# Kernel tuning notes

Hardware: AMD Instinct MI355X
Metric: run time of the kernel (lower is better)

Reference implementation:

```python
import jax, jax.numpy as jnp
import numpy as np

N_NODES = 100000
N_EDGES = 1600000
D_IN = 64
D_HID = 64


def setup_inputs() -> dict:
    key = jax.random.key(0)
    ks = jax.random.split(key, 9)
    feat = jax.random.uniform(ks[0], (N_NODES, D_IN), dtype=jnp.float32) + 1e-3
    edge_index = jax.random.randint(ks[1], (2, N_EDGES), 0, N_NODES, dtype=jnp.int64)
    edge_vals = jax.random.uniform(ks[2], (N_EDGES,), dtype=jnp.float32) + 1e-3
    W1 = jax.random.normal(ks[3], (D_IN, D_HID), dtype=jnp.float32) * 0.1
    b1 = jax.random.normal(ks[4], (D_HID,), dtype=jnp.float32) * 0.1
    W2 = jax.random.normal(ks[5], (D_HID, D_HID), dtype=jnp.float32) * 0.1
    b2 = jax.random.normal(ks[6], (D_HID,), dtype=jnp.float32) * 0.1
    W3 = jax.random.normal(ks[7], (D_HID, 1), dtype=jnp.float32) * 0.1
    b3 = jax.random.normal(ks[8], (1,), dtype=jnp.float32) * 0.1
    return {"feat": feat, "edge_index": edge_index, "edge_vals": edge_vals,
            "W1": W1, "b1": b1, "W2": W2, "b2": b2, "W3": W3, "b3": b3}


def reference(feat, edge_index, edge_vals, W1, b1, W2, b2, W3, b3):
    N = feat.shape[0]
    src = edge_index[0]
    dst = edge_index[1]
    # --- __init__: A_hat = D^{-1} A D^{-1}, D = diag(row sums of A) ---
    deg_row = jax.ops.segment_sum(edge_vals, src, num_segments=N)
    deg_row = jnp.where(deg_row > 0, deg_row, 1.0)  # guard isolated nodes
    w_hat = edge_vals / (deg_row[src] * deg_row[dst])  # A_hat edge weights
    # --- GCNConv gcn_norm: add self loops (weight 1), symmetric D^{-1/2} norm ---
    loops = jnp.arange(N, dtype=src.dtype)
    row = jnp.concatenate([src, loops])   # message sources
    col = jnp.concatenate([dst, loops])   # message targets (aggregation index)
    w = jnp.concatenate([w_hat, jnp.ones((N,), dtype=feat.dtype)])
    deg = jax.ops.segment_sum(w, col, num_segments=N)
    dinv = jnp.where(deg > 0, jax.lax.rsqrt(deg), 0.0)
    norm = dinv[row] * w * dinv[col]      # [E+N]

    def gcn_conv(x, W, b):
        h = x @ W                          # [N, d_out]
        msg = norm[:, None] * h[row]       # gather + scale, [E+N, d_out]
        return jax.ops.segment_sum(msg, col, num_segments=N) + b

    # --- forward ---
    x = feat / jnp.sum(feat, axis=1, keepdims=True)
    x = jax.nn.relu(gcn_conv(x, W1, b1))
    x = jax.nn.relu(gcn_conv(x, W2, b2))
    x = gcn_conv(x, W3, b3)               # final layer, no activation
    return x
```

## Files before the change

kernel.cpp:

```cpp
#include <hip/hip_runtime.h>
#include <hip/hip_fp16.h>


#define CAP    48
#define NRL    256
#define NBMX   512
#define P0E    2048

#define PG     2048

__device__ __forceinline__ float dec_ev(unsigned pk) {
    return __half2float(__ushort_as_half((unsigned short)(pk >> 17)));
}
__device__ __forceinline__ float dec_ev15(unsigned pk) {
    return __half2float(__ushort_as_half((unsigned short)(pk & 0x7FFF)));
}

__global__ __launch_bounds__(256) void k_scatter(
        const int* __restrict__ src, const int* __restrict__ dst,
        const float* __restrict__ ev,
        int* __restrict__ meta_d, int2* __restrict__ part_blk,
        int* __restrict__ meta_s, int* __restrict__ parts_src,
        int E, int NB) {
    __shared__ int2 srt[P0E];
    __shared__ int  srs[P0E];
    __shared__ int hd[NBMX], cbd[NBMX], lod[NBMX];
    __shared__ int hs[NBMX], cbs[NBMX], los[NBMX];
    int bx = (int)blockIdx.x, tid = (int)threadIdx.x;
    int e0 = bx * P0E;
    int ne = E - e0; if (ne > P0E) ne = P0E; if (ne < 0) ne = 0;
    for (int i = tid; i < NB; i += 256) { hd[i] = 0; hs[i] = 0; }
    __syncthreads();
    for (int i = tid; i < ne; i += 256) {
        atomicAdd(&hd[dst[e0 + i] >> 8], 1);
        atomicAdd(&hs[src[e0 + i] >> 8], 1);
    }
    __syncthreads();
    int wv = tid >> 6, ln = tid & 63;
    if (wv < 2) {
        int* h  = wv ? hs  : hd;
        int* cb = wv ? cbs : cbd;
        int run = 0;
        #pragma unroll
        for (int k = 0; k < NBMX / 64; k++) {
            int idx = k * 64 + ln;
            int v = (idx < NB) ? h[idx] : 0;
            int sc = v;
            #pragma unroll
            for (int o = 1; o < 64; o <<= 1) {
                int u = __shfl_up(sc, o, 64);
                if (ln >= o) sc += u;
            }
            if (idx < NB) cb[idx] = run + sc - v;
            run += __shfl(sc, 63, 64);
        }
    }
    __syncthreads();
    for (int c = tid; c < NB; c += 256) {
        lod[c] = cbd[c];
        los[c] = cbs[c];
        meta_d[(size_t)bx * NB + c] = (cbd[c] << 16) | hd[c];
        meta_s[(size_t)bx * NB + c] = (cbs[c] << 16) | hs[c];
    }
    __syncthreads();
    for (int i = tid; i < ne; i += 256) {
        int e = e0 + i;
        int s = src[e], d = dst[e];
        float v = ev[e];
        unsigned evh = (unsigned)__half_as_ushort(__float2half_rn(v)) & 0x7FFF;
        int p = atomicAdd(&lod[d >> 8], 1);
        int2 r;
        r.x = ((d & (NRL - 1)) << 17) | s;
        r.y = __float_as_int(v);
        srt[p] = r;
        int q = atomicAdd(&los[s >> 8], 1);
        srs[q] = (int)(((unsigned)(s & (NRL - 1)) << 15) | evh);
    }
    __syncthreads();
    for (int i = tid; i < ne; i += 256) {
        part_blk[(size_t)bx * P0E + i]  = srt[i];
        parts_src[(size_t)bx * P0E + i] = srs[i];
    }
}

__global__ __launch_bounds__(256) void k_degacc(
        const int* __restrict__ parts_src, const int* __restrict__ meta_s,
        float* __restrict__ deg_row, int N, int NB, int nsb) {
    __shared__ float dl[NRL];
    int b = (int)blockIdx.x, tid = (int)threadIdx.x;
    if (tid < NRL) dl[tid] = 0.f;
    __syncthreads();
    for (int bx = tid; bx < nsb; bx += 256) {
        int m = meta_s[(size_t)bx * NB + b];
        int base = m >> 16, len = m & 0xFFFF;
        const int* seg = parts_src + (size_t)bx * P0E + base;
        for (int j = 0; j < len; j++) {
            unsigned pk = (unsigned)seg[j];
            atomicAdd(&dl[pk >> 15], dec_ev15(pk));
        }
    }
    __syncthreads();
    int node = (b << 8) + tid;
    if (tid < NRL && node < N) deg_row[node] = dl[tid];
}

__global__ __launch_bounds__(256) void k_gemm1(
        const float* __restrict__ feat, const float* __restrict__ W1,
        __half* __restrict__ B, int N) {
    int lane = threadIdx.x & 63;
    float w[64];
    #pragma unroll
    for (int k = 0; k < 64; k++) w[k] = W1[k * 64 + lane];
    int wid = (int)blockIdx.x * 4 + (threadIdx.x >> 6);
    const int nw = PG * 4;
    for (int node = wid; node < N; node += nw) {
        float v = feat[(size_t)node * 64 + lane];
        float s = v;
        #pragma unroll
        for (int o = 1; o < 64; o <<= 1) s += __shfl_xor(s, o, 64);
        int myb = __float_as_int(v / s);
        float a0 = 0.f, a1 = 0.f, a2 = 0.f, a3 = 0.f;
        #pragma unroll
        for (int k = 0; k < 64; k += 4) {
            a0 = fmaf(__int_as_float(__builtin_amdgcn_readlane(myb, k + 0)), w[k + 0], a0);
            a1 = fmaf(__int_as_float(__builtin_amdgcn_readlane(myb, k + 1)), w[k + 1], a1);
            a2 = fmaf(__int_as_float(__builtin_amdgcn_readlane(myb, k + 2)), w[k + 2], a2);
            a3 = fmaf(__int_as_float(__builtin_amdgcn_readlane(myb, k + 3)), w[k + 3], a3);
        }
        B[(size_t)node * 64 + lane] = __float2half((a0 + a1) + (a2 + a3));
    }
}

__global__ __launch_bounds__(256) void k_bucket(
        const int2* __restrict__ part_blk, const int* __restrict__ meta_d,
        const float* __restrict__ deg_row,
        int* __restrict__ cnt, int* __restrict__ epair,
        float* __restrict__ di_t, float* __restrict__ r_t,
        int N, int NB, int nsb) {
    __shared__ int   lbuck[NRL * CAP];
    __shared__ int   lcnt[NRL];
    __shared__ float lt[NRL];
    int b = (int)blockIdx.x, tid = (int)threadIdx.x;
    if (tid < NRL) { lcnt[tid] = 0; lt[tid] = 0.f; }
    __syncthreads();
    for (int bx = tid; bx < nsb; bx += 256) {
        int m = meta_d[(size_t)bx * NB + b];
        int base = m >> 16, len = m & 0xFFFF;
        const int2* seg = part_blk + (size_t)bx * P0E + base;
        for (int j = 0; j < len; j++) {
            int2 r = seg[j];
            int dl = (r.x >> 17) & (NRL - 1);
            int s  = r.x & 0x1FFFF;
            float v = __int_as_float(r.y);
            atomicAdd(&lt[dl], v / deg_row[s]);
            unsigned evh = (unsigned)__half_as_ushort(__float2half_rn(v)) & 0x7FFF;
            int p = atomicAdd(&lcnt[dl], 1);
            if (p < CAP) lbuck[dl * CAP + p] = (int)((evh << 17) | (unsigned)s);
        }
    }
    __syncthreads();
    int node0 = b << 8;
    if (tid < NRL) {
        int node = node0 + tid;
        if (node < N) {
            int c = lcnt[tid]; if (c > CAP) c = CAP;
            cnt[node] = c;
            float drd = deg_row[node];
            drd = drd > 0.f ? drd : 1.f;
            float qd = 1.0f / drd;
            float di = rsqrtf(1.0f + qd * lt[tid]);
            di_t[node] = di;
            r_t[node]  = qd * di;
        }
    }
    __syncthreads();
    size_t base = (size_t)node0 * CAP;
    for (int i = tid; i < NRL * CAP; i += 256) epair[base + i] = lbuck[i];
}

__global__ __launch_bounds__(256) void k_p3(const int* __restrict__ cnt,
                                            int* __restrict__ epair,
                                            const float* __restrict__ r_t, int N) {
    int lane = threadIdx.x & 63;
    int node = blockIdx.x * 4 + (threadIdx.x >> 6);
    if (node >= N) return;
    int c = cnt[node]; if (c > CAP) c = CAP;
    if (lane < c) {
        size_t o = (size_t)node * CAP + lane;
        unsigned e = (unsigned)epair[o];
        int s = (int)(e & 0x1FFFF);
        float w = dec_ev(e) * r_t[s];
        unsigned wh = (unsigned)__half_as_ushort(__float2half_rn(w)) & 0x7FFF;
        epair[o] = (int)((wh << 17) | (unsigned)s);
    }
}

__device__ __forceinline__ void gt_fma8(const uint4& d, float w, float acc[8]) {
    const __half2* p = reinterpret_cast<const __half2*>(&d);
    #pragma unroll
    for (int q = 0; q < 4; q++) {
        float2 f = __half22float2(p[q]);
        acc[2 * q]     = fmaf(w, f.x, acc[2 * q]);
        acc[2 * q + 1] = fmaf(w, f.y, acc[2 * q + 1]);
    }
}

__device__ __forceinline__ void gt_block(int recr, int gb,
        const __half* __restrict__ hp, float acc[8]) {
    int e0 = __shfl(recr, gb + 0, 64);
    int e1 = __shfl(recr, gb + 1, 64);
    int e2 = __shfl(recr, gb + 2, 64);
    int e3 = __shfl(recr, gb + 3, 64);
    int e4 = __shfl(recr, gb + 4, 64);
    int e5 = __shfl(recr, gb + 5, 64);
    int e6 = __shfl(recr, gb + 6, 64);
    int e7 = __shfl(recr, gb + 7, 64);
    uint4 d0 = *reinterpret_cast<const uint4*>(hp + ((size_t)(e0 & 0x1FFFF) << 6));
    uint4 d1 = *reinterpret_cast<const uint4*>(hp + ((size_t)(e1 & 0x1FFFF) << 6));
    uint4 d2 = *reinterpret_cast<const uint4*>(hp + ((size_t)(e2 & 0x1FFFF) << 6));
    uint4 d3 = *reinterpret_cast<const uint4*>(hp + ((size_t)(e3 & 0x1FFFF) << 6));
    uint4 d4 = *reinterpret_cast<const uint4*>(hp + ((size_t)(e4 & 0x1FFFF) << 6));
    uint4 d5 = *reinterpret_cast<const uint4*>(hp + ((size_t)(e5 & 0x1FFFF) << 6));
    uint4 d6 = *reinterpret_cast<const uint4*>(hp + ((size_t)(e6 & 0x1FFFF) << 6));
    uint4 d7 = *reinterpret_cast<const uint4*>(hp + ((size_t)(e7 & 0x1FFFF) << 6));
    gt_fma8(d0, dec_ev((unsigned)e0), acc);
    gt_fma8(d1, dec_ev((unsigned)e1), acc);
    gt_fma8(d2, dec_ev((unsigned)e2), acc);
    gt_fma8(d3, dec_ev((unsigned)e3), acc);
    gt_fma8(d4, dec_ev((unsigned)e4), acc);
    gt_fma8(d5, dec_ev((unsigned)e5), acc);
    gt_fma8(d6, dec_ev((unsigned)e6), acc);
    gt_fma8(d7, dec_ev((unsigned)e7), acc);
}

#define GT_PROLOGUE(cntp, epairp)                                            \
    int lane = (int)threadIdx.x & 63;                                        \
    int grp = lane >> 3, sub = lane & 7;                                     \
    int base = (((int)blockIdx.x << 2) + ((int)threadIdx.x >> 6)) << 3;      \
    int un = base + grp;                                                     \
    int unc = un < N ? un : N - 1;                                           \
    int c = un < N ? cntp[unc] : 0;                                          \
    if (c > CAP) c = CAP;                                                    \
    const int* ep = epairp + (size_t)unc * CAP + sub;                        \
    int rec0 = 0, rec1 = 0, rec2 = 0, rec3 = 0, rec4 = 0, rec5 = 0;          \
    if (sub + 0  < c) rec0 = ep[0];                                          \
    if (sub + 8  < c) rec1 = ep[8];                                          \
    if (sub + 16 < c) rec2 = ep[16];                                         \
    if (sub + 24 < c) rec3 = ep[24];                                         \
    if (sub + 32 < c) rec4 = ep[32];                                         \
    if (sub + 40 < c) rec5 = ep[40];                                         \
    int m = c;                                                               \
    { int u;                                                                 \
      u = __shfl_xor(m, 8, 64);  m = m > u ? m : u;                          \
      u = __shfl_xor(m, 16, 64); m = m > u ? m : u;                          \
      u = __shfl_xor(m, 32, 64); m = m > u ? m : u; }                        \
    float acc[8];                                                            \
    _Pragma("unroll")                                                        \
    for (int q = 0; q < 8; q++) acc[q] = 0.f;                                \
    int gb = grp << 3;

__global__ __launch_bounds__(256) void k_gath1(
        const int* __restrict__ cnt, const int* __restrict__ epair,
        const __half* __restrict__ B,
        const float* __restrict__ di_t, const float* __restrict__ r_t,
        const float* __restrict__ b1, __half* __restrict__ X2, int N) {
    GT_PROLOGUE(cnt, epair)
    const __half* hp = B + (sub << 3);
    uint4 dow = *reinterpret_cast<const uint4*>(B + ((size_t)unc << 6) + (sub << 3));
    gt_block(rec0, gb, hp, acc);
    if (m > 8)  gt_block(rec1, gb, hp, acc);
    if (m > 16) gt_block(rec2, gb, hp, acc);
    if (m > 24) gt_block(rec3, gb, hp, acc);
    if (m > 32) gt_block(rec4, gb, hp, acc);
    if (m > 40) gt_block(rec5, gb, hp, acc);
    float di = di_t[unc], rd = r_t[unc];
    float dd = di * di;
    const float4* b4 = reinterpret_cast<const float4*>(b1);
    float4 bA = b4[sub * 2], bB = b4[sub * 2 + 1];
    const __half2* po = reinterpret_cast<const __half2*>(&dow);
    float2 o0 = __half22float2(po[0]), o1 = __half22float2(po[1]);
    float2 o2 = __half22float2(po[2]), o3 = __half22float2(po[3]);
    __half2 h0 = __floats2half2_rn(fmaxf(bA.x + dd * o0.x + rd * acc[0], 0.f),
                                   fmaxf(bA.y + dd * o0.y + rd * acc[1], 0.f));
    __half2 h1 = __floats2half2_rn(fmaxf(bA.z + dd * o1.x + rd * acc[2], 0.f),
                                   fmaxf(bA.w + dd * o1.y + rd * acc[3], 0.f));
    __half2 h2 = __floats2half2_rn(fmaxf(bB.x + dd * o2.x + rd * acc[4], 0.f),
                                   fmaxf(bB.y + dd * o2.y + rd * acc[5], 0.f));
    __half2 h3 = __floats2half2_rn(fmaxf(bB.z + dd * o3.x + rd * acc[6], 0.f),
                                   fmaxf(bB.w + dd * o3.y + rd * acc[7], 0.f));
    if (un < N) {
        uint4 ov;
        ov.x = *reinterpret_cast<unsigned*>(&h0);
        ov.y = *reinterpret_cast<unsigned*>(&h1);
        ov.z = *reinterpret_cast<unsigned*>(&h2);
        ov.w = *reinterpret_cast<unsigned*>(&h3);
        *reinterpret_cast<uint4*>(X2 + ((size_t)un << 6) + (sub << 3)) = ov;
    }
}

__global__ __launch_bounds__(256) void k_gemm2(
        const __half* __restrict__ X2, const float* __restrict__ W2,
        __half* __restrict__ C, int N) {
    int lane = threadIdx.x & 63;
    float w[64];
    #pragma unroll
    for (int k = 0; k < 64; k++) w[k] = W2[k * 64 + lane];
    int wid = (int)blockIdx.x * 4 + (threadIdx.x >> 6);
    const int nw = PG * 4;
    for (int node = wid; node < N; node += nw) {
        int myb = __float_as_int(__half2float(X2[(size_t)node * 64 + lane]));
        float a0 = 0.f, a1 = 0.f, a2 = 0.f, a3 = 0.f;
        #pragma unroll
        for (int k = 0; k < 64; k += 4) {
            a0 = fmaf(__int_as_float(__builtin_amdgcn_readlane(myb, k + 0)), w[k + 0], a0);
            a1 = fmaf(__int_as_float(__builtin_amdgcn_readlane(myb, k + 1)), w[k + 1], a1);
            a2 = fmaf(__int_as_float(__builtin_amdgcn_readlane(myb, k + 2)), w[k + 2], a2);
            a3 = fmaf(__int_as_float(__builtin_amdgcn_readlane(myb, k + 3)), w[k + 3], a3);
        }
        C[(size_t)node * 64 + lane] = __float2half((a0 + a1) + (a2 + a3));
    }
}

__global__ __launch_bounds__(256) void k_gather_dot(
        const int* __restrict__ cnt, const int* __restrict__ epair,
        const __half* __restrict__ C,
        const float* __restrict__ di_t, const float* __restrict__ r_t,
        const float* __restrict__ b2, const float* __restrict__ W3,
        float* __restrict__ h3, int N) {
    GT_PROLOGUE(cnt, epair)
    const __half* hp = C + (sub << 3);
    uint4 dow = *reinterpret_cast<const uint4*>(C + ((size_t)unc << 6) + (sub << 3));
    gt_block(rec0, gb, hp, acc);
    if (m > 8)  gt_block(rec1, gb, hp, acc);
    if (m > 16) gt_block(rec2, gb, hp, acc);
    if (m > 24) gt_block(rec3, gb, hp, acc);
    if (m > 32) gt_block(rec4, gb, hp, acc);
    if (m > 40) gt_block(rec5, gb, hp, acc);
    float di = di_t[unc], rd = r_t[unc];
    float dd = di * di;
    const float4* b4 = reinterpret_cast<const float4*>(b2);
    const float4* w4 = reinterpret_cast<const float4*>(W3);
    float4 bA = b4[sub * 2], bB = b4[sub * 2 + 1];
    float4 wA = w4[sub * 2], wB = w4[sub * 2 + 1];
    const __half2* po = reinterpret_cast<const __half2*>(&dow);
    float2 o0 = __half22float2(po[0]), o1 = __half22float2(po[1]);
    float2 o2 = __half22float2(po[2]), o3 = __half22float2(po[3]);
    float pd = 0.f;
    pd += fmaxf(bA.x + dd * o0.x + rd * acc[0], 0.f) * wA.x;
    pd += fmaxf(bA.y + dd * o0.y + rd * acc[1], 0.f) * wA.y;
    pd += fmaxf(bA.z + dd * o1.x + rd * acc[2], 0.f) * wA.z;
    pd += fmaxf(bA.w + dd * o1.y + rd * acc[3], 0.f) * wA.w;
    pd += fmaxf(bB.x + dd * o2.x + rd * acc[4], 0.f) * wB.x;
    pd += fmaxf(bB.y + dd * o2.y + rd * acc[5], 0.f) * wB.y;
    pd += fmaxf(bB.z + dd * o3.x + rd * acc[6], 0.f) * wB.z;
    pd += fmaxf(bB.w + dd * o3.y + rd * acc[7], 0.f) * wB.w;
    pd += __shfl_xor(pd, 1, 64);
    pd += __shfl_xor(pd, 2, 64);
    pd += __shfl_xor(pd, 4, 64);
    if (sub == 0 && un < N) h3[un] = pd;
}

__global__ __launch_bounds__(256) void k_gather1(const int* __restrict__ cnt,
                                                 const int* __restrict__ epair,
                                                 const float* __restrict__ h3,
                                                 const float* __restrict__ di_t,
                                                 const float* __restrict__ r_t,
                                                 const float* __restrict__ b3,
                                                 float* __restrict__ out, int N) {
    int lane = threadIdx.x & 63;
    int node = blockIdx.x * 4 + (threadIdx.x >> 6);
    if (node >= N) return;
    int c = cnt[node]; if (c > CAP) c = CAP;
    float e0 = 0.f;
    if (lane < c) {
        unsigned pk = (unsigned)epair[(size_t)node * CAP + lane];
        e0 = dec_ev(pk) * h3[pk & 0x1FFFF];
    }
    #pragma unroll
    for (int o = 1; o < 64; o <<= 1) e0 += __shfl_xor(e0, o, 64);
    if (lane == 0) {
        float di = di_t[node];
        out[node] = b3[0] + di * di * h3[node] + r_t[node] * e0;
    }
}

extern "C" void kernel_launch(void* const* d_in, const int* in_sizes, int n_in,
                              void* d_out, int out_size, void* d_ws, size_t ws_size,
                              hipStream_t stream) {
    const float* feat = (const float*)d_in[0];
    const int*   eidx = (const int*)d_in[1];
    const float* ev   = (const float*)d_in[2];
    const float* W1 = (const float*)d_in[3];
    const float* b1 = (const float*)d_in[4];
    const float* W2 = (const float*)d_in[5];
    const float* b2 = (const float*)d_in[6];
    const float* W3 = (const float*)d_in[7];
    const float* b3 = (const float*)d_in[8];

    const int N = in_sizes[0] / 64;
    const int E = in_sizes[2];
    const int* src = eidx;
    const int* dst = eidx + E;
    const int NB   = (N + NRL - 1) / NRL;
    const int npad = NB * NRL;
    const int nsb  = (E + P0E - 1) / P0E;

    char* p = (char*)d_ws;
    auto carve = [&](size_t nbytes) { char* r = p; p += (nbytes + 255) & ~(size_t)255; return r; };
    float*    deg_row   = (float*)   carve((size_t)N * 4);
    float*    di_t      = (float*)   carve((size_t)N * 4);
    float*    r_t       = (float*)   carve((size_t)N * 4);
    float*    h3        = (float*)   carve((size_t)N * 4);
    int*      cnt       = (int*)     carve((size_t)npad * 4);
    int*      meta_d    = (int*)     carve((size_t)nsb * NB * 4);
    int*      meta_s    = (int*)     carve((size_t)nsb * NB * 4);
    int*      epair     = (int*)     carve((size_t)npad * CAP * 4);
    int2*     part_blk  = (int2*)    carve((size_t)nsb * P0E * 8);
    int*      parts_src = (int*)     carve((size_t)nsb * P0E * 4);
    __half*   B         = (__half*)  carve((size_t)N * 64 * 2);
    __half*   X2        = (__half*)part_blk;
    __half*   C         = (__half*)B;
    float*    out       = (float*)d_out;

    const int BLK = 256;
    int gNode4  = (N + 3) / 4;
    int gNode32 = (N + 31) / 32;

    k_scatter   <<<nsb, BLK, 0, stream>>>(src, dst, ev, meta_d, part_blk,
                                          meta_s, parts_src, E, NB);
    k_degacc    <<<NB, BLK, 0, stream>>>(parts_src, meta_s, deg_row, N, NB, nsb);
    k_gemm1     <<<PG, BLK, 0, stream>>>(feat, W1, B, N);
    k_bucket    <<<NB, BLK, 0, stream>>>(part_blk, meta_d, deg_row, cnt, epair,
                                         di_t, r_t, N, NB, nsb);
    k_p3        <<<gNode4, BLK, 0, stream>>>(cnt, epair, r_t, N);

    k_gath1     <<<gNode32, BLK, 0, stream>>>(cnt, epair, B, di_t, r_t, b1, X2, N);
    k_gemm2     <<<PG, BLK, 0, stream>>>(X2, W2, C, N);
    k_gather_dot<<<gNode32, BLK, 0, stream>>>(cnt, epair, C, di_t, r_t,
                                              b2, W3, h3, N);
    k_gather1   <<<gNode4, BLK, 0, stream>>>(cnt, epair, h3, di_t, r_t, b3, out, N);
}
```

Baseline: 305.0 us.

## Merge scatter with gemm1 launch and fold r_t weighting into gathers

The edge scatter and the first feature GEMM now run as one launch, with block indices split by role, so the two independent jobs overlap and one launch is saved. The k_p3 pass that rewrote each edge weight as ev*r_t[src] is removed. Each gather kernel now applies that factor on the fly when it reads an edge record, which costs an extra random r_t load per edge in each of three layers. The merged kernel still reserves the scatter's large shared memory and the gemm's 64-float register array for every block, which may lower occupancy.

Result: faster. 292.7 us (-4.0%).

```diff
diff --git a/kernel.cpp b/kernel.cpp
--- a/kernel.cpp
+++ b/kernel.cpp
@@ -16,70 +16,104 @@
     return __half2float(__ushort_as_half((unsigned short)(pk & 0x7FFF)));
 }
 
-__global__ __launch_bounds__(256) void k_scatter(
+__device__ __forceinline__ int fold_rt(int rec, const float* __restrict__ rt) {
+    int s = rec & 0x1FFFF;
+    float w = dec_ev((unsigned)rec) * rt[s];
+    unsigned wh = (unsigned)__half_as_ushort(__float2half_rn(w)) & 0x7FFF;
+    return (int)((wh << 17) | (unsigned)s);
+}
+
+__global__ __launch_bounds__(256) void k_p0(
         const int* __restrict__ src, const int* __restrict__ dst,
         const float* __restrict__ ev,
         int* __restrict__ meta_d, int2* __restrict__ part_blk,
         int* __restrict__ meta_s, int* __restrict__ parts_src,
-        int E, int NB) {
+        const float* __restrict__ feat, const float* __restrict__ W1,
+        __half* __restrict__ B, int E, int N, int NB, int nsb) {
     __shared__ int2 srt[P0E];
     __shared__ int  srs[P0E];
     __shared__ int hd[NBMX], cbd[NBMX], lod[NBMX];
     __shared__ int hs[NBMX], cbs[NBMX], los[NBMX];
     int bx = (int)blockIdx.x, tid = (int)threadIdx.x;
-    int e0 = bx * P0E;
-    int ne = E - e0; if (ne > P0E) ne = P0E; if (ne < 0) ne = 0;
-    for (int i = tid; i < NB; i += 256) { hd[i] = 0; hs[i] = 0; }
-    __syncthreads();
-    for (int i = tid; i < ne; i += 256) {
-        atomicAdd(&hd[dst[e0 + i] >> 8], 1);
-        atomicAdd(&hs[src[e0 + i] >> 8], 1);
-    }
-    __syncthreads();
-    int wv = tid >> 6, ln = tid & 63;
-    if (wv < 2) {
-        int* h  = wv ? hs  : hd;
-        int* cb = wv ? cbs : cbd;
-        int run = 0;
+    if (bx < nsb) {
+        int e0 = bx * P0E;
+        int ne = E - e0; if (ne > P0E) ne = P0E; if (ne < 0) ne = 0;
+        for (int i = tid; i < NB; i += 256) { hd[i] = 0; hs[i] = 0; }
+        __syncthreads();
+        for (int i = tid; i < ne; i += 256) {
+            atomicAdd(&hd[dst[e0 + i] >> 8], 1);
+            atomicAdd(&hs[src[e0 + i] >> 8], 1);
+        }
+        __syncthreads();
+        int wv = tid >> 6, ln = tid & 63;
+        if (wv < 2) {
+            int* h  = wv ? hs  : hd;
+            int* cb = wv ? cbs : cbd;
+            int run = 0;
+            #pragma unroll
+            for (int k = 0; k < NBMX / 64; k++) {
+                int idx = k * 64 + ln;
+                int v = (idx < NB) ? h[idx] : 0;
+                int sc = v;
+                #pragma unroll
+                for (int o = 1; o < 64; o <<= 1) {
+                    int u = __shfl_up(sc, o, 64);
+                    if (ln >= o) sc += u;
+                }
+                if (idx < NB) cb[idx] = run + sc - v;
+                run += __shfl(sc, 63, 64);
+            }
+        }
+        __syncthreads();
+        for (int c = tid; c < NB; c += 256) {
+            lod[c] = cbd[c];
+            los[c] = cbs[c];
+            meta_d[(size_t)bx * NB + c] = (cbd[c] << 16) | hd[c];
+            meta_s[(size_t)bx * NB + c] = (cbs[c] << 16) | hs[c];
+        }
+        __syncthreads();
+        for (int i = tid; i < ne; i += 256) {
+            int e = e0 + i;
+            int s = src[e], d = dst[e];
+            float v = ev[e];
+            unsigned evh = (unsigned)__half_as_ushort(__float2half_rn(v)) & 0x7FFF;
+            int p = atomicAdd(&lod[d >> 8], 1);
+            int2 r;
+            r.x = ((d & (NRL - 1)) << 17) | s;
+            r.y = __float_as_int(v);
+            srt[p] = r;
+            int q = atomicAdd(&los[s >> 8], 1);
+            srs[q] = (int)(((unsigned)(s & (NRL - 1)) << 15) | evh);
+        }
+        __syncthreads();
+        for (int i = tid; i < ne; i += 256) {
+            part_blk[(size_t)bx * P0E + i]  = srt[i];
+            parts_src[(size_t)bx * P0E + i] = srs[i];
+        }
+        return;
+    }
+    bx -= nsb;
+    int lane = tid & 63;
+    float w[64];
+    #pragma unroll
+    for (int k = 0; k < 64; k++) w[k] = W1[k * 64 + lane];
+    int wid = bx * 4 + (tid >> 6);
+    const int nw = PG * 4;
+    for (int node = wid; node < N; node += nw) {
+        float v = feat[(size_t)node * 64 + lane];
+        float s = v;
         #pragma unroll
-        for (int k = 0; k < NBMX / 64; k++) {
-            int idx = k * 64 + ln;
-            int v = (idx < NB) ? h[idx] : 0;
-            int sc = v;
-            #pragma unroll
-            for (int o = 1; o < 64; o <<= 1) {
-                int u = __shfl_up(sc, o, 64);
-                if (ln >= o) sc += u;
-            }
-            if (idx < NB) cb[idx] = run + sc - v;
-            run += __shfl(sc, 63, 64);
-        }
-    }
-    __syncthreads();
-    for (int c = tid; c < NB; c += 256) {
-        lod[c] = cbd[c];
-        los[c] = cbs[c];
-        meta_d[(size_t)bx * NB + c] = (cbd[c] << 16) | hd[c];
-        meta_s[(size_t)bx * NB + c] = (cbs[c] << 16) | hs[c];
-    }
-    __syncthreads();
-    for (int i = tid; i < ne; i += 256) {
-        int e = e0 + i;
-        int s = src[e], d = dst[e];
-        float v = ev[e];
-        unsigned evh = (unsigned)__half_as_ushort(__float2half_rn(v)) & 0x7FFF;
-        int p = atomicAdd(&lod[d >> 8], 1);
-        int2 r;
-        r.x = ((d & (NRL - 1)) << 17) | s;
-        r.y = __float_as_int(v);
-        srt[p] = r;
-        int q = atomicAdd(&los[s >> 8], 1);
-        srs[q] = (int)(((unsigned)(s & (NRL - 1)) << 15) | evh);
-    }
-    __syncthreads();
-    for (int i = tid; i < ne; i += 256) {
-        part_blk[(size_t)bx * P0E + i]  = srt[i];
-        parts_src[(size_t)bx * P0E + i] = srs[i];
+        for (int o = 1; o < 64; o <<= 1) s += __shfl_xor(s, o, 64);
+        int myb = __float_as_int(v / s);
+        float a0 = 0.f, a1 = 0.f, a2 = 0.f, a3 = 0.f;
+        #pragma unroll
+        for (int k = 0; k < 64; k += 4) {
+            a0 = fmaf(__int_as_float(__builtin_amdgcn_readlane(myb, k + 0)), w[k + 0], a0);
+            a1 = fmaf(__int_as_float(__builtin_amdgcn_readlane(myb, k + 1)), w[k + 1], a1);
+            a2 = fmaf(__int_as_float(__builtin_amdgcn_readlane(myb, k + 2)), w[k + 2], a2);
+            a3 = fmaf(__int_as_float(__builtin_amdgcn_readlane(myb, k + 3)), w[k + 3], a3);
+        }
+        B[(size_t)node * 64 + lane] = __float2half((a0 + a1) + (a2 + a3));
     }
 }
 
@@ -102,33 +136,6 @@
     __syncthreads();
     int node = (b << 8) + tid;
     if (tid < NRL && node < N) deg_row[node] = dl[tid];
-}
-
-__global__ __launch_bounds__(256) void k_gemm1(
-        const float* __restrict__ feat, const float* __restrict__ W1,
-        __half* __restrict__ B, int N) {
-    int lane = threadIdx.x & 63;
-    float w[64];
-    #pragma unroll
-    for (int k = 0; k < 64; k++) w[k] = W1[k * 64 + lane];
-    int wid = (int)blockIdx.x * 4 + (threadIdx.x >> 6);
-    const int nw = PG * 4;
-    for (int node = wid; node < N; node += nw) {
-        float v = feat[(size_t)node * 64 + lane];
-        float s = v;
-        #pragma unroll
-        for (int o = 1; o < 64; o <<= 1) s += __shfl_xor(s, o, 64);
-        int myb = __float_as_int(v / s);
-        float a0 = 0.f, a1 = 0.f, a2 = 0.f, a3 = 0.f;
-        #pragma unroll
-        for (int k = 0; k < 64; k += 4) {
-            a0 = fmaf(__int_as_float(__builtin_amdgcn_readlane(myb, k + 0)), w[k + 0], a0);
-            a1 = fmaf(__int_as_float(__builtin_amdgcn_readlane(myb, k + 1)), w[k + 1], a1);
-            a2 = fmaf(__int_as_float(__builtin_amdgcn_readlane(myb, k + 2)), w[k + 2], a2);
-            a3 = fmaf(__int_as_float(__builtin_amdgcn_readlane(myb, k + 3)), w[k + 3], a3);
-        }
-        B[(size_t)node * 64 + lane] = __float2half((a0 + a1) + (a2 + a3));
-    }
 }
 
 __global__ __launch_bounds__(256) void k_bucket(
@@ -176,23 +183,6 @@
     __syncthreads();
     size_t base = (size_t)node0 * CAP;
     for (int i = tid; i < NRL * CAP; i += 256) epair[base + i] = lbuck[i];
-}
-
-__global__ __launch_bounds__(256) void k_p3(const int* __restrict__ cnt,
-                                            int* __restrict__ epair,
-                                            const float* __restrict__ r_t, int N) {
-    int lane = threadIdx.x & 63;
-    int node = blockIdx.x * 4 + (threadIdx.x >> 6);
-    if (node >= N) return;
-    int c = cnt[node]; if (c > CAP) c = CAP;
-    if (lane < c) {
-        size_t o = (size_t)node * CAP + lane;
-        unsigned e = (unsigned)epair[o];
-        int s = (int)(e & 0x1FFFF);
-        float w = dec_ev(e) * r_t[s];
-        unsigned wh = (unsigned)__half_as_ushort(__float2half_rn(w)) & 0x7FFF;
-        epair[o] = (int)((wh << 17) | (unsigned)s);
-    }
 }
 
 __device__ __forceinline__ void gt_fma8(const uint4& d, float w, float acc[8]) {
@@ -233,7 +223,7 @@
     gt_fma8(d7, dec_ev((unsigned)e7), acc);
 }
 
-#define GT_PROLOGUE(cntp, epairp)                                            \
+#define GT_PROLOGUE(cntp, epairp, rtp)                                       \
     int lane = (int)threadIdx.x & 63;                                        \
     int grp = lane >> 3, sub = lane & 7;                                     \
     int base = (((int)blockIdx.x << 2) + ((int)threadIdx.x >> 6)) << 3;      \
@@ -249,6 +239,12 @@
     if (sub + 24 < c) rec3 = ep[24];                                         \
     if (sub + 32 < c) rec4 = ep[32];                                         \
     if (sub + 40 < c) rec5 = ep[40];                                         \
+    rec0 = fold_rt(rec0, rtp);                                               \
+    rec1 = fold_rt(rec1, rtp);                                               \
+    rec2 = fold_rt(rec2, rtp);                                               \
+    rec3 = fold_rt(rec3, rtp);                                               \
+    rec4 = fold_rt(rec4, rtp);                                               \
+    rec5 = fold_rt(rec5, rtp);                                               \
     int m = c;                                                               \
     { int u;                                                                 \
       u = __shfl_xor(m, 8, 64);  m = m > u ? m : u;                          \
@@ -264,7 +260,7 @@
         const __half* __restrict__ B,
         const float* __restrict__ di_t, const float* __restrict__ r_t,
         const float* __restrict__ b1, __half* __restrict__ X2, int N) {
-    GT_PROLOGUE(cnt, epair)
+    GT_PROLOGUE(cnt, epair, r_t)
     const __half* hp = B + (sub << 3);
     uint4 dow = *reinterpret_cast<const uint4*>(B + ((size_t)unc << 6) + (sub << 3));
     gt_block(rec0, gb, hp, acc);
@@ -327,7 +323,7 @@
         const float* __restrict__ di_t, const float* __restrict__ r_t,
         const float* __restrict__ b2, const float* __restrict__ W3,
         float* __restrict__ h3, int N) {
-    GT_PROLOGUE(cnt, epair)
+    GT_PROLOGUE(cnt, epair, r_t)
     const __half* hp = C + (sub << 3);
     uint4 dow = *reinterpret_cast<const uint4*>(C + ((size_t)unc << 6) + (sub << 3));
     gt_block(rec0, gb, hp, acc);
@@ -374,7 +370,8 @@
     float e0 = 0.f;
     if (lane < c) {
         unsigned pk = (unsigned)epair[(size_t)node * CAP + lane];
-        e0 = dec_ev(pk) * h3[pk & 0x1FFFF];
+        int s = (int)(pk & 0x1FFFF);
+        e0 = dec_ev(pk) * r_t[s] * h3[s];
     }
     #pragma unroll
     for (int o = 1; o < 64; o <<= 1) e0 += __shfl_xor(e0, o, 64);
@@ -426,13 +423,12 @@
     int gNode4  = (N + 3) / 4;
     int gNode32 = (N + 31) / 32;
 
-    k_scatter   <<<nsb, BLK, 0, stream>>>(src, dst, ev, meta_d, part_blk,
-                                          meta_s, parts_src, E, NB);
+    k_p0        <<<nsb + PG, BLK, 0, stream>>>(src, dst, ev, meta_d, part_blk,
+                                               meta_s, parts_src, feat, W1, B,
+                                               E, N, NB, nsb);
     k_degacc    <<<NB, BLK, 0, stream>>>(parts_src, meta_s, deg_row, N, NB, nsb);
-    k_gemm1     <<<PG, BLK, 0, stream>>>(feat, W1, B, N);
     k_bucket    <<<NB, BLK, 0, stream>>>(part_blk, meta_d, deg_row, cnt, epair,
                                          di_t, r_t, N, NB, nsb);
-    k_p3        <<<gNode4, BLK, 0, stream>>>(cnt, epair, r_t, N);
 
     k_gath1     <<<gNode32, BLK, 0, stream>>>(cnt, epair, B, di_t, r_t, b1, X2, N);
     k_gemm2     <<<PG, BLK, 0, stream>>>(X2, W2, C, N);
```
